# Kernel optimization log

Hardware: AMD Instinct MI355X
Metric: run time of the kernel (lower is better)

Reference implementation:

```python
import jax, jax.numpy as jnp
import numpy as np

B, D, R, E, L = 16384, 1024, 64, 4, 3


def setup_inputs() -> dict:
    key = jax.random.key(0)
    ks = jax.random.split(key, 6)
    x0 = jax.random.normal(ks[0], (B, D), dtype=jnp.float32)
    # Expert low-rank factors: U projects D->R, V projects R->D (both bias-free)
    U = jax.random.normal(ks[1], (L, E, D, R), dtype=jnp.float32) * (1.0 / np.sqrt(D))
    V = jax.random.normal(ks[2], (L, E, R, D), dtype=jnp.float32) * (1.0 / np.sqrt(R))
    # Gate Linear(D, E) with bias
    gW = jax.random.normal(ks[3], (L, D, E), dtype=jnp.float32) * (1.0 / np.sqrt(D))
    gb = jax.random.normal(ks[4], (L, E), dtype=jnp.float32) * 0.01
    # Per-layer bias added after mixing (initialized zeros in torch; small random here)
    bias = jax.random.normal(ks[5], (L, D), dtype=jnp.float32) * 0.01
    return {"x0": x0, "U": U, "V": V, "gW": gW, "gb": gb, "bias": bias}


def reference(x0, U, V, gW, gb, bias):
    x = x0
    for l in range(L):
        # batched low-rank expert MLPs: [B,D] -> [B,E,R] -> relu -> [B,E,D]
        h = jax.nn.relu(jnp.einsum('bd,edr->ber', x, U[l]))
        expert_out = jnp.einsum('ber,erd->bed', h, V[l])
        # soft gate over experts
        gate = jax.nn.softmax(x @ gW[l] + gb[l], axis=-1)  # [B,E]
        mixed = jnp.einsum('be,bed->bd', gate, expert_out)  # [B,D]
        x = x0 * mixed + bias[l] + x
    return x
```

## Files before the change

### kernel.cpp

```cpp
#include <hip/hip_runtime.h>

#define DEVI __device__ __forceinline__

typedef __bf16 bf16x8 __attribute__((ext_vector_type(8)));
typedef float f32x4 __attribute__((ext_vector_type(4)));
typedef unsigned short u16x8 __attribute__((ext_vector_type(8)));

DEVI unsigned short f2bf(float f) {
  unsigned u = __builtin_bit_cast(unsigned, f);
  u += 0x7FFFu + ((u >> 16) & 1u);
  return (unsigned short)(u >> 16);
}
DEVI float bf2f(unsigned short h) {
  return __builtin_bit_cast(float, (unsigned)h << 16);
}

__global__ __launch_bounds__(256) void prep_kernel(const float* __restrict__ x,
                                                   const float* __restrict__ U,
                                                   const float* __restrict__ V,
                                                   const float* __restrict__ gW,
                                                   unsigned short* __restrict__ xb,
                                                   unsigned short* __restrict__ W1T,
                                                   unsigned short* __restrict__ V2T,
                                                   unsigned short* __restrict__ gWT) {
  int b = blockIdx.x;
  if (b < 8192) {
    int i = b * 256 + threadIdx.x;
    const f32x4* p = (const f32x4*)x;
    f32x4 a = p[2 * i], b2 = p[2 * i + 1];
    u16x8 o;
    o[0] = f2bf(a[0]); o[1] = f2bf(a[1]); o[2] = f2bf(a[2]); o[3] = f2bf(a[3]);
    o[4] = f2bf(b2[0]); o[5] = f2bf(b2[1]); o[6] = f2bf(b2[2]); o[7] = f2bf(b2[3]);
    ((u16x8*)xb)[i] = o;
  } else if (b < 11264) {
    int idx = (b - 8192) * 256 + threadIdx.x;
    int l = idx >> 18;
    int rem = idx & 262143;
    int n = rem >> 10, k = rem & 1023;
    int e = n >> 6, r = n & 63;
    W1T[idx] = f2bf(U[(size_t)(((l * 4 + e) << 10) + k) * 64 + r]);
  } else if (b < 14336) {
    int idx = (b - 11264) * 256 + threadIdx.x;
    int l = idx >> 18;
    int rem = idx & 262143;
    int d = rem >> 8, c = rem & 255;
    int e = c >> 6, r = c & 63;
    V2T[idx] = f2bf(V[(size_t)(((l * 4 + e) * 64 + r) << 10) + d]);
  } else {
    int idx = (b - 14336) * 256 + threadIdx.x;
    int l = idx >> 14;
    int n = (idx >> 10) & 15;
    int k = idx & 1023;
    float v = (n < 4) ? gW[l * 4096 + k * 4 + n] : 0.0f;
    gWT[idx] = f2bf(v);
  }
}

__global__ __launch_bounds__(256) void k1_kernel(const unsigned short* __restrict__ A,
                                                 const unsigned short* __restrict__ Bw,
                                                 const unsigned short* __restrict__ gWT,
                                                 const float* __restrict__ gb,
                                                 unsigned short* __restrict__ Hg) {
  constexpr int K = 1024;
  __shared__ char lds[20480];
  __shared__ float gls[128];
  int t = threadIdx.x;
  int wid = t >> 6, lane = t & 63;
  int g4 = lane >> 4, l15 = lane & 15;
  int wm = wid >> 1, wn = wid & 1;

  int j = blockIdx.x;
  int s = j >> 3;
  int p = (j & 7) * 64 + (s >> 1);
  int ybl = s & 1;
  int m0 = p * 32, n0 = ybl * 128;

  int srow = t >> 3;
  int scolb = ((t & 7) * 16) ^ ((srow & 7) << 4);
  const unsigned short* Asrc = A + (size_t)(m0 + srow) * K + (scolb >> 1);
  const unsigned short* Bsrc = Bw + (size_t)(n0 + srow) * K + (scolb >> 1);

  f32x4 acc[4], accg;
  {
    f32x4 z = {0.f, 0.f, 0.f, 0.f};
    accg = z;
#pragma unroll
    for (int n = 0; n < 4; ++n) acc[n] = z;
  }

  for (int ks = 0; ks < K; ks += 64) {
    __syncthreads();
    __builtin_amdgcn_global_load_lds(
        (const __attribute__((address_space(1))) void*)(Asrc + ks),
        (__attribute__((address_space(3))) void*)(lds + wid * 1024), 16, 0, 0);
#pragma unroll
    for (int i = 0; i < 4; ++i)
      __builtin_amdgcn_global_load_lds(
          (const __attribute__((address_space(1))) void*)(Bsrc + (size_t)i * 32 * K + ks),
          (__attribute__((address_space(3))) void*)(lds + 4096 + i * 4096 + wid * 1024), 16, 0, 0);
    __syncthreads();
#pragma unroll
    for (int kk = 0; kk < 2; ++kk) {
      bf16x8 af;
      {
        int row = wm * 16 + l15;
        af = *(const bf16x8*)(lds + row * 128 + ((kk * 64 + g4 * 16) ^ ((row & 7) << 4)));
      }
      bf16x8 gf;
      if (wn == 0) gf = *(const bf16x8*)(gWT + (size_t)l15 * 1024 + ks + kk * 32 + g4 * 8);
#pragma unroll
      for (int n = 0; n < 4; ++n) {
        int row = wn * 64 + n * 16 + l15;
        bf16x8 bfr = *(const bf16x8*)(lds + 4096 + row * 128 +
                                      ((kk * 64 + g4 * 16) ^ ((row & 7) << 4)));
        acc[n] = __builtin_amdgcn_mfma_f32_16x16x32_bf16(af, bfr, acc[n], 0, 0, 0);
      }
      if (wn == 0)
        accg = __builtin_amdgcn_mfma_f32_16x16x32_bf16(af, gf, accg, 0, 0, 0);
    }
  }

  if (wn == 0) {
    float gbv = gb[l15 & 3];
#pragma unroll
    for (int jj = 0; jj < 4; ++jj) {
      float v = accg[jj] + gbv;
      float mx = fmaxf(v, __shfl_xor(v, 1));
      mx = fmaxf(mx, __shfl_xor(mx, 2));
      float ev = __expf(v - mx);
      float sm = ev + __shfl_xor(ev, 1);
      sm += __shfl_xor(sm, 2);
      if (l15 < 4) gls[(wm * 16 + g4 * 4 + jj) * 4 + l15] = ev / sm;
    }
  }
  __syncthreads();

  int e = ybl * 2 + wn;
#pragma unroll
  for (int n = 0; n < 4; ++n) {
#pragma unroll
    for (int jj = 0; jj < 4; ++jj) {
      int row = wm * 16 + g4 * 4 + jj;
      int col = wn * 64 + n * 16 + l15;
      float v = fmaxf(acc[n][jj], 0.f) * gls[row * 4 + e];
      *(unsigned short*)(lds + 4096 + row * 256 + ((col * 2) ^ ((row & 7) << 4))) = f2bf(v);
    }
  }
  __syncthreads();

#pragma unroll
  for (int i = 0; i < 2; ++i) {
    int row = i * 16 + (t >> 4);
    int seg = (t & 15) * 16;
    u16x8 v = *(const u16x8*)(lds + 4096 + row * 256 + (seg ^ ((row & 7) << 4)));
    *(u16x8*)(Hg + (size_t)(m0 + row) * 256 + n0 + (seg >> 1)) = v;
  }
}

__global__ __launch_bounds__(256) void k2_kernel(const unsigned short* __restrict__ A,
                                                 const unsigned short* __restrict__ Bw,
                                                 const unsigned short* __restrict__ x0b,
                                                 const float* __restrict__ x0f,
                                                 const unsigned short* __restrict__ xcur,
                                                 const float* __restrict__ biasl,
                                                 unsigned short* __restrict__ xnext,
                                                 float* __restrict__ out,
                                                 int last, int use_x0b, int same_x) {
  constexpr int K = 256;
  __shared__ char lds[20480];
  int t = threadIdx.x;
  int wid = t >> 6, lane = t & 63;
  int g4 = lane >> 4, l15 = lane & 15;
  int wm = wid >> 1, wn = wid & 1;

  int j = blockIdx.x;
  int s = j >> 3;
  int xbl = (j & 7) * 64 + (s >> 3);
  int ybl = s & 7;
  int m0 = xbl * 32, n0 = ybl * 128;

  int srow = t >> 3;
  int scolb = ((t & 7) * 16) ^ ((srow & 7) << 4);
  const unsigned short* Asrc = A + (size_t)(m0 + srow) * K + (scolb >> 1);
  const unsigned short* Bsrc = Bw + (size_t)(n0 + srow) * K + (scolb >> 1);

  f32x4 acc[4];
#pragma unroll
  for (int n = 0; n < 4; ++n) { f32x4 z = {0.f, 0.f, 0.f, 0.f}; acc[n] = z; }

  for (int ks = 0; ks < K; ks += 64) {
    __syncthreads();
    __builtin_amdgcn_global_load_lds(
        (const __attribute__((address_space(1))) void*)(Asrc + ks),
        (__attribute__((address_space(3))) void*)(lds + wid * 1024), 16, 0, 0);
#pragma unroll
    for (int i = 0; i < 4; ++i)
      __builtin_amdgcn_global_load_lds(
          (const __attribute__((address_space(1))) void*)(Bsrc + (size_t)i * 32 * K + ks),
          (__attribute__((address_space(3))) void*)(lds + 4096 + i * 4096 + wid * 1024), 16, 0, 0);
    __syncthreads();
#pragma unroll
    for (int kk = 0; kk < 2; ++kk) {
      bf16x8 af;
      {
        int row = wm * 16 + l15;
        af = *(const bf16x8*)(lds + row * 128 + ((kk * 64 + g4 * 16) ^ ((row & 7) << 4)));
      }
#pragma unroll
      for (int n = 0; n < 4; ++n) {
        int row = wn * 64 + n * 16 + l15;
        bf16x8 bfr = *(const bf16x8*)(lds + 4096 + row * 128 +
                                      ((kk * 64 + g4 * 16) ^ ((row & 7) << 4)));
        acc[n] = __builtin_amdgcn_mfma_f32_16x16x32_bf16(af, bfr, acc[n], 0, 0, 0);
      }
    }
  }
  __syncthreads();

#pragma unroll
  for (int n = 0; n < 4; ++n) {
#pragma unroll
    for (int jj = 0; jj < 4; ++jj) {
      int row = wm * 16 + g4 * 4 + jj;
      int col = wn * 64 + n * 16 + l15;
      *(unsigned short*)(lds + 4096 + row * 256 + ((col * 2) ^ ((row & 7) << 4))) =
          f2bf(acc[n][jj]);
    }
  }
  __syncthreads();

#pragma unroll
  for (int i = 0; i < 2; ++i) {
    int row = i * 16 + (t >> 4);
    int seg = (t & 15) * 16;
    u16x8 a8 = *(const u16x8*)(lds + 4096 + row * 256 + (seg ^ ((row & 7) << 4)));
    size_t goff = (size_t)(m0 + row) * 1024 + n0 + (seg >> 1);
    u16x8 cv = *(const u16x8*)(xcur + goff);
    float x0v[8];
    if (same_x) {
#pragma unroll
      for (int k = 0; k < 8; ++k) x0v[k] = bf2f(cv[k]);
    } else if (use_x0b) {
      u16x8 xv = *(const u16x8*)(x0b + goff);
#pragma unroll
      for (int k = 0; k < 8; ++k) x0v[k] = bf2f(xv[k]);
    } else {
      f32x4 xa = *(const f32x4*)(x0f + goff);
      f32x4 xb2 = *(const f32x4*)(x0f + goff + 4);
#pragma unroll
      for (int k = 0; k < 4; ++k) { x0v[k] = xa[k]; x0v[k + 4] = xb2[k]; }
    }
    const float* bp = biasl + n0 + (seg >> 1);
    f32x4 b0 = *(const f32x4*)bp;
    f32x4 b1 = *(const f32x4*)(bp + 4);
    float r[8];
#pragma unroll
    for (int k = 0; k < 8; ++k) {
      float bv = (k < 4) ? b0[k & 3] : b1[k & 3];
      r[k] = x0v[k] * bf2f(a8[k]) + bv + bf2f(cv[k]);
    }
    if (last) {
      f32x4 r0, r1;
#pragma unroll
      for (int k = 0; k < 4; ++k) { r0[k] = r[k]; r1[k] = r[k + 4]; }
      *(f32x4*)(out + goff) = r0;
      *(f32x4*)(out + goff + 4) = r1;
    } else {
      u16x8 o;
#pragma unroll
      for (int k = 0; k < 8; ++k) o[k] = f2bf(r[k]);
      *(u16x8*)(xnext + goff) = o;
    }
  }
}

extern "C" void kernel_launch(void* const* d_in, const int* in_sizes, int n_in,
                              void* d_out, int out_size, void* d_ws, size_t ws_size,
                              hipStream_t stream) {
  const float* x0 = (const float*)d_in[0];
  const float* U = (const float*)d_in[1];
  const float* V = (const float*)d_in[2];
  const float* gW = (const float*)d_in[3];
  const float* gb = (const float*)d_in[4];
  const float* bias = (const float*)d_in[5];
  float* out = (float*)d_out;
  char* ws = (char*)d_ws;

  const size_t SZ_X = 33554432;
  const size_t SZ_HG = 8388608;
  const size_t SZ_W = 1572864;
  const size_t SZ_GW = 98304;
  bool use_x0b = ws_size >= (2 * SZ_X + SZ_HG + 2 * SZ_W + SZ_GW);

  size_t off = 0;
  unsigned short* x0b = nullptr;
  if (use_x0b) { x0b = (unsigned short*)(ws + off); off += SZ_X; }
  unsigned short* xbf = (unsigned short*)(ws + off); off += SZ_X;
  unsigned short* hg = (unsigned short*)(ws + off); off += SZ_HG;
  unsigned short* W1T = (unsigned short*)(ws + off); off += SZ_W;
  unsigned short* V2T = (unsigned short*)(ws + off); off += SZ_W;
  unsigned short* gWT = (unsigned short*)(ws + off); off += SZ_GW;

  unsigned short* xinit = use_x0b ? x0b : xbf;

  prep_kernel<<<14528, 256, 0, stream>>>(x0, U, V, gW, xinit, W1T, V2T, gWT);

  for (int l = 0; l < 3; ++l) {
    const unsigned short* xs = (l == 0) ? xinit : xbf;
    int same_x = (l == 0 && use_x0b) ? 1 : 0;
    k1_kernel<<<1024, 256, 0, stream>>>(xs, W1T + l * 262144, gWT + l * 16384,
                                        gb + l * 4, hg);
    k2_kernel<<<4096, 256, 0, stream>>>(hg, V2T + l * 262144,
                                        use_x0b ? x0b : nullptr, x0, xs,
                                        bias + l * 1024, xbf, out,
                                        (l == 2) ? 1 : 0, use_x0b ? 1 : 0, same_x);
  }
}
```

Measured before the change: 168.8 us.

## Fuse per-layer expert up-projection, gating and down-projection into one kernel

Replaces the two per-layer kernels (x·U with gate/softmax writing Hg, then Hg·V with residual epilogue) with one 512-thread kernel. Each block computes a 32-row tile of the full 256-wide gated hidden activation, keeps it in LDS, and loops over four 256-column output chunks for the down-projection and epilogue. This removes the Hg round trip through global memory and one launch per layer. In exchange the grid drops to 512 blocks, LDS use per block is much larger, which may lower occupancy, and the down-projection runs serially over the output chunks inside each block.

```diff
diff --git a/kernel.cpp b/kernel.cpp
--- a/kernel.cpp
+++ b/kernel.cpp
@@ -1,6 +1,8 @@
 #include <hip/hip_runtime.h>
 
 #define DEVI __device__ __forceinline__
+#define AS1 const __attribute__((address_space(1))) void*
+#define AS3 __attribute__((address_space(3))) void*
 
 typedef __bf16 bf16x8 __attribute__((ext_vector_type(8)));
 typedef float f32x4 __attribute__((ext_vector_type(4)));
@@ -56,220 +58,211 @@
   }
 }
 
-__global__ __launch_bounds__(256) void k1_kernel(const unsigned short* __restrict__ A,
-                                                 const unsigned short* __restrict__ Bw,
-                                                 const unsigned short* __restrict__ gWT,
-                                                 const float* __restrict__ gb,
-                                                 unsigned short* __restrict__ Hg) {
-  constexpr int K = 1024;
-  __shared__ char lds[20480];
-  __shared__ float gls[128];
+__global__ __launch_bounds__(512) void layer_kernel(
+    const unsigned short* __restrict__ xsrc,
+    const unsigned short* __restrict__ W1T,
+    const unsigned short* __restrict__ V2T,
+    const unsigned short* __restrict__ gWT,
+    const float* __restrict__ gb,
+    const float* __restrict__ biasl,
+    const unsigned short* __restrict__ x0b,
+    const float* __restrict__ x0f,
+    unsigned short* __restrict__ xnext,
+    float* __restrict__ out,
+    int last, int use_x0b, int same_x) {
+  __shared__ char lds[53760];
+  float* gls = (float*)(lds + 53248);
   int t = threadIdx.x;
-  int wid = t >> 6, lane = t & 63;
+  int w = t >> 6, lane = t & 63;
   int g4 = lane >> 4, l15 = lane & 15;
-  int wm = wid >> 1, wn = wid & 1;
 
   int j = blockIdx.x;
-  int s = j >> 3;
-  int p = (j & 7) * 64 + (s >> 1);
-  int ybl = s & 1;
-  int m0 = p * 32, n0 = ybl * 128;
-
-  int srow = t >> 3;
-  int scolb = ((t & 7) * 16) ^ ((srow & 7) << 4);
-  const unsigned short* Asrc = A + (size_t)(m0 + srow) * K + (scolb >> 1);
-  const unsigned short* Bsrc = Bw + (size_t)(n0 + srow) * K + (scolb >> 1);
-
-  f32x4 acc[4], accg;
+  int p = (j & 7) * 64 + (j >> 3);
+  int m0 = p * 32;
+
+  int srow8 = t >> 3;
+  int scolb = ((t & 7) * 16) ^ ((srow8 & 7) << 4);
+  const unsigned short* Asrc = xsrc + (size_t)(m0 + srow8) * 1024 + (scolb >> 1);
+  const unsigned short* B1src = W1T + (size_t)srow8 * 1024 + (scolb >> 1);
+
+  f32x4 acc[2][2], accg[2];
   {
     f32x4 z = {0.f, 0.f, 0.f, 0.f};
-    accg = z;
-#pragma unroll
-    for (int n = 0; n < 4; ++n) acc[n] = z;
-  }
-
-  for (int ks = 0; ks < K; ks += 64) {
+    accg[0] = z; accg[1] = z;
+#pragma unroll
+    for (int m = 0; m < 2; ++m)
+#pragma unroll
+      for (int n = 0; n < 2; ++n) acc[m][n] = z;
+  }
+
+  for (int ks = 0; ks < 1024; ks += 64) {
     __syncthreads();
-    __builtin_amdgcn_global_load_lds(
-        (const __attribute__((address_space(1))) void*)(Asrc + ks),
-        (__attribute__((address_space(3))) void*)(lds + wid * 1024), 16, 0, 0);
+    if (t < 256)
+      __builtin_amdgcn_global_load_lds((AS1)(Asrc + ks), (AS3)(lds + w * 1024), 16, 0, 0);
 #pragma unroll
     for (int i = 0; i < 4; ++i)
       __builtin_amdgcn_global_load_lds(
-          (const __attribute__((address_space(1))) void*)(Bsrc + (size_t)i * 32 * K + ks),
-          (__attribute__((address_space(3))) void*)(lds + 4096 + i * 4096 + wid * 1024), 16, 0, 0);
+          (AS1)(B1src + (size_t)i * 64 * 1024 + ks),
+          (AS3)(lds + 4096 + i * 8192 + w * 1024), 16, 0, 0);
     __syncthreads();
 #pragma unroll
     for (int kk = 0; kk < 2; ++kk) {
-      bf16x8 af;
-      {
-        int row = wm * 16 + l15;
-        af = *(const bf16x8*)(lds + row * 128 + ((kk * 64 + g4 * 16) ^ ((row & 7) << 4)));
+      int kb = kk * 64 + g4 * 16;
+      bf16x8 af[2];
+#pragma unroll
+      for (int m = 0; m < 2; ++m) {
+        int row = m * 16 + l15;
+        af[m] = *(const bf16x8*)(lds + row * 128 + (kb ^ ((row & 7) << 4)));
       }
       bf16x8 gf;
-      if (wn == 0) gf = *(const bf16x8*)(gWT + (size_t)l15 * 1024 + ks + kk * 32 + g4 * 8);
-#pragma unroll
-      for (int n = 0; n < 4; ++n) {
-        int row = wn * 64 + n * 16 + l15;
-        bf16x8 bfr = *(const bf16x8*)(lds + 4096 + row * 128 +
-                                      ((kk * 64 + g4 * 16) ^ ((row & 7) << 4)));
-        acc[n] = __builtin_amdgcn_mfma_f32_16x16x32_bf16(af, bfr, acc[n], 0, 0, 0);
-      }
-      if (wn == 0)
-        accg = __builtin_amdgcn_mfma_f32_16x16x32_bf16(af, gf, accg, 0, 0, 0);
-    }
-  }
-
-  if (wn == 0) {
+      if (w == 0) gf = *(const bf16x8*)(gWT + (size_t)l15 * 1024 + ks + kk * 32 + g4 * 8);
+#pragma unroll
+      for (int n = 0; n < 2; ++n) {
+        int row = w * 32 + n * 16 + l15;
+        bf16x8 bfr = *(const bf16x8*)(lds + 4096 + row * 128 + (kb ^ ((row & 7) << 4)));
+#pragma unroll
+        for (int m = 0; m < 2; ++m)
+          acc[m][n] = __builtin_amdgcn_mfma_f32_16x16x32_bf16(af[m], bfr, acc[m][n], 0, 0, 0);
+      }
+      if (w == 0) {
+#pragma unroll
+        for (int m = 0; m < 2; ++m)
+          accg[m] = __builtin_amdgcn_mfma_f32_16x16x32_bf16(af[m], gf, accg[m], 0, 0, 0);
+      }
+    }
+  }
+
+  if (w == 0) {
     float gbv = gb[l15 & 3];
 #pragma unroll
-    for (int jj = 0; jj < 4; ++jj) {
-      float v = accg[jj] + gbv;
-      float mx = fmaxf(v, __shfl_xor(v, 1));
-      mx = fmaxf(mx, __shfl_xor(mx, 2));
-      float ev = __expf(v - mx);
-      float sm = ev + __shfl_xor(ev, 1);
-      sm += __shfl_xor(sm, 2);
-      if (l15 < 4) gls[(wm * 16 + g4 * 4 + jj) * 4 + l15] = ev / sm;
+    for (int m = 0; m < 2; ++m) {
+#pragma unroll
+      for (int jj = 0; jj < 4; ++jj) {
+        float v = accg[m][jj] + gbv;
+        float mx = fmaxf(v, __shfl_xor(v, 1));
+        mx = fmaxf(mx, __shfl_xor(mx, 2));
+        float ev = __expf(v - mx);
+        float sm = ev + __shfl_xor(ev, 1);
+        sm += __shfl_xor(sm, 2);
+        if (l15 < 4) gls[(m * 16 + g4 * 4 + jj) * 4 + l15] = ev / sm;
+      }
     }
   }
   __syncthreads();
 
-  int e = ybl * 2 + wn;
-#pragma unroll
-  for (int n = 0; n < 4; ++n) {
-#pragma unroll
-    for (int jj = 0; jj < 4; ++jj) {
-      int row = wm * 16 + g4 * 4 + jj;
-      int col = wn * 64 + n * 16 + l15;
-      float v = fmaxf(acc[n][jj], 0.f) * gls[row * 4 + e];
-      *(unsigned short*)(lds + 4096 + row * 256 + ((col * 2) ^ ((row & 7) << 4))) = f2bf(v);
+#pragma unroll
+  for (int m = 0; m < 2; ++m) {
+#pragma unroll
+    for (int n = 0; n < 2; ++n) {
+#pragma unroll
+      for (int jj = 0; jj < 4; ++jj) {
+        int row = m * 16 + g4 * 4 + jj;
+        int col = w * 32 + n * 16 + l15;
+        float v = fmaxf(acc[m][n][jj], 0.f) * gls[row * 4 + (col >> 6)];
+        *(unsigned short*)(lds + 36864 + row * 512 + ((col * 2) ^ ((row & 7) << 4))) = f2bf(v);
+      }
     }
   }
   __syncthreads();
 
-#pragma unroll
-  for (int i = 0; i < 2; ++i) {
-    int row = i * 16 + (t >> 4);
-    int seg = (t & 15) * 16;
-    u16x8 v = *(const u16x8*)(lds + 4096 + row * 256 + (seg ^ ((row & 7) << 4)));
-    *(u16x8*)(Hg + (size_t)(m0 + row) * 256 + n0 + (seg >> 1)) = v;
-  }
-}
-
-__global__ __launch_bounds__(256) void k2_kernel(const unsigned short* __restrict__ A,
-                                                 const unsigned short* __restrict__ Bw,
-                                                 const unsigned short* __restrict__ x0b,
-                                                 const float* __restrict__ x0f,
-                                                 const unsigned short* __restrict__ xcur,
-                                                 const float* __restrict__ biasl,
-                                                 unsigned short* __restrict__ xnext,
-                                                 float* __restrict__ out,
-                                                 int last, int use_x0b, int same_x) {
-  constexpr int K = 256;
-  __shared__ char lds[20480];
-  int t = threadIdx.x;
-  int wid = t >> 6, lane = t & 63;
-  int g4 = lane >> 4, l15 = lane & 15;
-  int wm = wid >> 1, wn = wid & 1;
-
-  int j = blockIdx.x;
-  int s = j >> 3;
-  int xbl = (j & 7) * 64 + (s >> 3);
-  int ybl = s & 7;
-  int m0 = xbl * 32, n0 = ybl * 128;
-
-  int srow = t >> 3;
-  int scolb = ((t & 7) * 16) ^ ((srow & 7) << 4);
-  const unsigned short* Asrc = A + (size_t)(m0 + srow) * K + (scolb >> 1);
-  const unsigned short* Bsrc = Bw + (size_t)(n0 + srow) * K + (scolb >> 1);
-
-  f32x4 acc[4];
-#pragma unroll
-  for (int n = 0; n < 4; ++n) { f32x4 z = {0.f, 0.f, 0.f, 0.f}; acc[n] = z; }
-
-  for (int ks = 0; ks < K; ks += 64) {
+  for (int nc = 0; nc < 4; ++nc) {
+    f32x4 acc2[2][2];
+    {
+      f32x4 z = {0.f, 0.f, 0.f, 0.f};
+#pragma unroll
+      for (int m = 0; m < 2; ++m)
+#pragma unroll
+        for (int n = 0; n < 2; ++n) acc2[m][n] = z;
+    }
+    for (int ks2 = 0; ks2 < 256; ks2 += 64) {
+      __syncthreads();
+#pragma unroll
+      for (int i = 0; i < 4; ++i)
+        __builtin_amdgcn_global_load_lds(
+            (AS1)(V2T + (size_t)(nc * 256 + i * 64 + srow8) * 256 + ks2 + (scolb >> 1)),
+            (AS3)(lds + 4096 + i * 8192 + w * 1024), 16, 0, 0);
+      __syncthreads();
+#pragma unroll
+      for (int kk = 0; kk < 2; ++kk) {
+        int kb = kk * 64 + g4 * 16;
+        int kcol = ks2 + kk * 32 + g4 * 8;
+        bf16x8 af[2];
+#pragma unroll
+        for (int m = 0; m < 2; ++m) {
+          int row = m * 16 + l15;
+          af[m] = *(const bf16x8*)(lds + 36864 + row * 512 + ((kcol * 2) ^ ((row & 7) << 4)));
+        }
+#pragma unroll
+        for (int n = 0; n < 2; ++n) {
+          int row = w * 32 + n * 16 + l15;
+          bf16x8 bfr = *(const bf16x8*)(lds + 4096 + row * 128 + (kb ^ ((row & 7) << 4)));
+#pragma unroll
+          for (int m = 0; m < 2; ++m)
+            acc2[m][n] = __builtin_amdgcn_mfma_f32_16x16x32_bf16(af[m], bfr, acc2[m][n], 0, 0, 0);
+        }
+      }
+    }
+
     __syncthreads();
-    __builtin_amdgcn_global_load_lds(
-        (const __attribute__((address_space(1))) void*)(Asrc + ks),
-        (__attribute__((address_space(3))) void*)(lds + wid * 1024), 16, 0, 0);
-#pragma unroll
-    for (int i = 0; i < 4; ++i)
-      __builtin_amdgcn_global_load_lds(
-          (const __attribute__((address_space(1))) void*)(Bsrc + (size_t)i * 32 * K + ks),
-          (__attribute__((address_space(3))) void*)(lds + 4096 + i * 4096 + wid * 1024), 16, 0, 0);
+#pragma unroll
+    for (int m = 0; m < 2; ++m) {
+#pragma unroll
+      for (int n = 0; n < 2; ++n) {
+#pragma unroll
+        for (int jj = 0; jj < 4; ++jj) {
+          int row = m * 16 + g4 * 4 + jj;
+          int col = w * 32 + n * 16 + l15;
+          *(unsigned short*)(lds + 4096 + row * 512 + ((col * 2) ^ ((row & 7) << 4))) =
+              f2bf(acc2[m][n][jj]);
+        }
+      }
+    }
     __syncthreads();
-#pragma unroll
-    for (int kk = 0; kk < 2; ++kk) {
-      bf16x8 af;
-      {
-        int row = wm * 16 + l15;
-        af = *(const bf16x8*)(lds + row * 128 + ((kk * 64 + g4 * 16) ^ ((row & 7) << 4)));
-      }
-#pragma unroll
-      for (int n = 0; n < 4; ++n) {
-        int row = wn * 64 + n * 16 + l15;
-        bf16x8 bfr = *(const bf16x8*)(lds + 4096 + row * 128 +
-                                      ((kk * 64 + g4 * 16) ^ ((row & 7) << 4)));
-        acc[n] = __builtin_amdgcn_mfma_f32_16x16x32_bf16(af, bfr, acc[n], 0, 0, 0);
-      }
-    }
-  }
-  __syncthreads();
-
-#pragma unroll
-  for (int n = 0; n < 4; ++n) {
-#pragma unroll
-    for (int jj = 0; jj < 4; ++jj) {
-      int row = wm * 16 + g4 * 4 + jj;
-      int col = wn * 64 + n * 16 + l15;
-      *(unsigned short*)(lds + 4096 + row * 256 + ((col * 2) ^ ((row & 7) << 4))) =
-          f2bf(acc[n][jj]);
-    }
-  }
-  __syncthreads();
-
-#pragma unroll
-  for (int i = 0; i < 2; ++i) {
-    int row = i * 16 + (t >> 4);
-    int seg = (t & 15) * 16;
-    u16x8 a8 = *(const u16x8*)(lds + 4096 + row * 256 + (seg ^ ((row & 7) << 4)));
-    size_t goff = (size_t)(m0 + row) * 1024 + n0 + (seg >> 1);
-    u16x8 cv = *(const u16x8*)(xcur + goff);
-    float x0v[8];
-    if (same_x) {
-#pragma unroll
-      for (int k = 0; k < 8; ++k) x0v[k] = bf2f(cv[k]);
-    } else if (use_x0b) {
-      u16x8 xv = *(const u16x8*)(x0b + goff);
-#pragma unroll
-      for (int k = 0; k < 8; ++k) x0v[k] = bf2f(xv[k]);
-    } else {
-      f32x4 xa = *(const f32x4*)(x0f + goff);
-      f32x4 xb2 = *(const f32x4*)(x0f + goff + 4);
-#pragma unroll
-      for (int k = 0; k < 4; ++k) { x0v[k] = xa[k]; x0v[k + 4] = xb2[k]; }
-    }
-    const float* bp = biasl + n0 + (seg >> 1);
-    f32x4 b0 = *(const f32x4*)bp;
-    f32x4 b1 = *(const f32x4*)(bp + 4);
-    float r[8];
-#pragma unroll
-    for (int k = 0; k < 8; ++k) {
-      float bv = (k < 4) ? b0[k & 3] : b1[k & 3];
-      r[k] = x0v[k] * bf2f(a8[k]) + bv + bf2f(cv[k]);
-    }
-    if (last) {
-      f32x4 r0, r1;
-#pragma unroll
-      for (int k = 0; k < 4; ++k) { r0[k] = r[k]; r1[k] = r[k + 4]; }
-      *(f32x4*)(out + goff) = r0;
-      *(f32x4*)(out + goff + 4) = r1;
-    } else {
-      u16x8 o;
-#pragma unroll
-      for (int k = 0; k < 8; ++k) o[k] = f2bf(r[k]);
-      *(u16x8*)(xnext + goff) = o;
+    {
+      int row = t >> 4;
+      int seg0 = (t & 15) * 32;
+#pragma unroll
+      for (int h = 0; h < 2; ++h) {
+        int sb = seg0 + h * 16;
+        u16x8 a8 = *(const u16x8*)(lds + 4096 + row * 512 + (sb ^ ((row & 7) << 4)));
+        size_t goff = (size_t)(m0 + row) * 1024 + nc * 256 + (sb >> 1);
+        u16x8 cv = *(const u16x8*)(xsrc + goff);
+        float x0v[8];
+        if (same_x) {
+#pragma unroll
+          for (int k = 0; k < 8; ++k) x0v[k] = bf2f(cv[k]);
+        } else if (use_x0b) {
+          u16x8 xv = *(const u16x8*)(x0b + goff);
+#pragma unroll
+          for (int k = 0; k < 8; ++k) x0v[k] = bf2f(xv[k]);
+        } else {
+          f32x4 xa = *(const f32x4*)(x0f + goff);
+          f32x4 xb2 = *(const f32x4*)(x0f + goff + 4);
+#pragma unroll
+          for (int k = 0; k < 4; ++k) { x0v[k] = xa[k]; x0v[k + 4] = xb2[k]; }
+        }
+        const float* bp = biasl + nc * 256 + (sb >> 1);
+        f32x4 b0 = *(const f32x4*)bp;
+        f32x4 b1 = *(const f32x4*)(bp + 4);
+        float r[8];
+#pragma unroll
+        for (int k = 0; k < 8; ++k) {
+          float bv = (k < 4) ? b0[k & 3] : b1[k & 3];
+          r[k] = x0v[k] * bf2f(a8[k]) + bv + bf2f(cv[k]);
+        }
+        if (last) {
+          f32x4 r0, r1;
+#pragma unroll
+          for (int k = 0; k < 4; ++k) { r0[k] = r[k]; r1[k] = r[k + 4]; }
+          *(f32x4*)(out + goff) = r0;
+          *(f32x4*)(out + goff + 4) = r1;
+        } else {
+          u16x8 o;
+#pragma unroll
+          for (int k = 0; k < 8; ++k) o[k] = f2bf(r[k]);
+          *(u16x8*)(xnext + goff) = o;
+        }
+      }
     }
   }
 }
@@ -296,7 +289,7 @@
   unsigned short* x0b = nullptr;
   if (use_x0b) { x0b = (unsigned short*)(ws + off); off += SZ_X; }
   unsigned short* xbf = (unsigned short*)(ws + off); off += SZ_X;
-  unsigned short* hg = (unsigned short*)(ws + off); off += SZ_HG;
+  off += SZ_HG;
   unsigned short* W1T = (unsigned short*)(ws + off); off += SZ_W;
   unsigned short* V2T = (unsigned short*)(ws + off); off += SZ_W;
   unsigned short* gWT = (unsigned short*)(ws + off); off += SZ_GW;
@@ -308,11 +301,9 @@
   for (int l = 0; l < 3; ++l) {
     const unsigned short* xs = (l == 0) ? xinit : xbf;
     int same_x = (l == 0 && use_x0b) ? 1 : 0;
-    k1_kernel<<<1024, 256, 0, stream>>>(xs, W1T + l * 262144, gWT + l * 16384,
-                                        gb + l * 4, hg);
-    k2_kernel<<<4096, 256, 0, stream>>>(hg, V2T + l * 262144,
-                                        use_x0b ? x0b : nullptr, x0, xs,
-                                        bias + l * 1024, xbf, out,
-                                        (l == 2) ? 1 : 0, use_x0b ? 1 : 0, same_x);
-  }
-}
+    layer_kernel<<<512, 512, 0, stream>>>(xs, W1T + l * 262144, V2T + l * 262144,
+                                          gWT + l * 16384, gb + l * 4, bias + l * 1024,
+                                          x0b, x0, xbf, out,
+                                          (l == 2) ? 1 : 0, use_x0b ? 1 : 0, same_x);
+  }
+}
```

Result: slower. 184.2 us (+9.1%).
